# Kernel tuning notes

Measured on AMD Instinct MI355X. Metric: run time of the kernel, lower is better.

Reference implementation:

```python
import jax, jax.numpy as jnp
from jax import lax
import numpy as np

NUM_FEATURES = 30_000_000
NB_LABELS = 11  # 9 real tags + BOS + EOS
BOS, EOS = 9, 10
SEQ_LEN = 8192
N_ACTIVE = 14


def _make_transitions(key):
    t = jax.random.uniform(key, (NB_LABELS, NB_LABELS), minval=-0.1, maxval=0.1, dtype=jnp.float32)
    # hardcoded structural constraints from init_weights
    t = t.at[0:3, 4].set(-10.0).at[4:, 4].set(-10.0)
    t = t.at[0:1, 6].set(-10.0).at[2:, 6].set(-10.0)
    t = t.at[0:2, 7].set(-10.0).at[3:, 7].set(-10.0)
    t = t.at[0:5, 8].set(-10.0).at[6:, 8].set(-10.0)
    t = t.at[:, BOS].set(-10000.0)
    t = t.at[EOS, :].set(-10000.0)
    return t


def setup_inputs() -> dict:
    key = jax.random.key(0)
    k1, k2, k3 = jax.random.split(key, 3)
    x = jax.random.randint(k1, (SEQ_LEN, NB_LABELS, N_ACTIVE), 0, NUM_FEATURES, dtype=jnp.int64)
    # original inits emission weights to exactly 1.0; add tiny noise for a non-degenerate test
    emission_w = 1.0 + 0.01 * jax.random.normal(k2, (NUM_FEATURES,), dtype=jnp.float32)
    transitions = _make_transitions(k3)
    return {"x": x, "emission_w": emission_w, "transitions": transitions}


def reference(x, emission_w, transitions):
    # emissions: sparse feature-hashing sum == gather + sum over the 14 active indices
    emissions = emission_w[x].sum(-1)[None]  # (1, T, NB_LABELS)

    alphas0 = transitions[BOS][None] + emissions[:, 0]  # (1, L)

    def step(alphas, e_t):  # e_t: (1, L)
        # scores[b, prev, cur] = alphas[b, prev] + transitions[prev, cur] + e_t[b, cur]
        scores = alphas[:, :, None] + transitions[None] + e_t[:, None, :]
        return jnp.max(scores, axis=1), jnp.argmax(scores, axis=1)

    xs = jnp.swapaxes(emissions, 0, 1)[1:]  # (T-1, 1, L)
    alphas, bps = lax.scan(step, alphas0, xs)  # bps: (T-1, 1, L)

    end_scores = alphas + transitions[:, EOS][None]
    max_final_scores = jnp.max(end_scores, axis=1)  # (1,)
    final_tag = jnp.argmax(end_scores, axis=1)  # (1,)

    def back(tag, bp):  # tag: (1,), bp: (1, L)
        prev = bp[0][tag]
        return prev, prev

    _, earlier = lax.scan(back, final_tag, bps, reverse=True)  # (T-1, 1); earlier[t] = tag at time t
    path = jnp.concatenate([earlier[:, 0], final_tag])  # (T,)

    # sequential BIO-style path fixup, carrying the *corrected* previous tag
    def fix(prev, cur):
        new = cur
        new = jnp.where((cur == 4) & (prev != 3) & (prev != 4), 3, new)
        new = jnp.where((cur == 6) & (prev != 1) & (prev != 6), 1, new)
        new = jnp.where((cur == 7) & (prev != 2) & (prev != 7), 2, new)
        new = jnp.where((cur == 8) & (prev != 5) & (prev != 8), 5, new)
        return new, new

    _, fixed = lax.scan(fix, path[0], path[1:])
    path = jnp.concatenate([path[:1], fixed])
    return max_final_scores, path
```

## Files before the change

### kernel.cpp

```cpp
#include <hip/hip_runtime.h>
#include <stdint.h>


#define SEQ 8192
#define L 11
#define NS 9
#define NACT 14
#define NCH 128
#define CS 64

#define RL(v, l) __int_as_float(__builtin_amdgcn_readlane(__float_as_int(v), (l)))

#define OFF_E9 0
#define OFF_M 295040
#define OFF_BD 336512
#define OFF_AL 341184
#define OFF_DUMP 341248
#define OFF_BP 342272

__global__ __launch_bounds__(256) void k_emissions(const int* __restrict__ x,
                                                   const float* __restrict__ w,
                                                   float* __restrict__ E9) {
  int idx = blockIdx.x * 256 + threadIdx.x;
  int t = idx / 9;
  int c = idx - t * 9;
  const int* xr = x + (t * L + c) * NACT;
  int id[NACT];
#pragma unroll
  for (int j = 0; j < 7; j++) {
    int2 v = ((const int2*)xr)[j];
    id[2 * j] = v.x;
    id[2 * j + 1] = v.y;
  }
  float wv[NACT];
#pragma unroll
  for (int j = 0; j < NACT; j++) wv[j] = w[id[j]];
  float s = ((wv[0] + wv[1]) + (wv[2] + wv[3])) + ((wv[4] + wv[5]) + (wv[6] + wv[7]));
  s += wv[8]; s += wv[9]; s += wv[10]; s += wv[11]; s += wv[12]; s += wv[13];
  E9[idx] = s;
}

__global__ __launch_bounds__(64) void k_chunkmat(const float* __restrict__ E9,
                                                 const float* __restrict__ T,
                                                 float* __restrict__ M) {
  const int k = blockIdx.x;
  const int i = threadIdx.x;
  const int ii = (i < NS) ? i : (NS - 1);
  const bool act = (i < NS);

  float Tm[NS][NS];
#pragma unroll
  for (int p = 0; p < NS; p++)
#pragma unroll
    for (int c = 0; c < NS; c++) Tm[p][c] = T[p * L + c];

  const int t0 = k * CS + 1;
  const int len = (k == NCH - 1) ? (CS - 1) : CS;
  const float* ep = E9 + t0 * NS;

  float row[NS];
  {
    float e0[NS];
#pragma unroll
    for (int c = 0; c < NS; c++) e0[c] = ep[c];
#pragma unroll
    for (int c = 0; c < NS; c++) row[c] = Tm[ii][c] + e0[c];
  }
  float ebuf[NS];
#pragma unroll
  for (int c = 0; c < NS; c++) ebuf[c] = ep[NS + c];

#pragma unroll 2
  for (int r = 1; r < len; ++r) {
    float nrow[NS];
#pragma unroll
    for (int c = 0; c < NS; c++) {
      float s0 = row[0] + Tm[0][c];
      float s1 = row[1] + Tm[1][c];
      float s2 = row[2] + Tm[2][c];
      float s3 = row[3] + Tm[3][c];
      float s4 = row[4] + Tm[4][c];
      float s5 = row[5] + Tm[5][c];
      float s6 = row[6] + Tm[6][c];
      float s7 = row[7] + Tm[7][c];
      float s8 = row[8] + Tm[8][c];
      float ma = fmaxf(fmaxf(s0, s1), s2);
      float mb = fmaxf(fmaxf(s3, s4), s5);
      float mc = fmaxf(fmaxf(s6, s7), s8);
      nrow[c] = fmaxf(fmaxf(ma, mb), mc) + ebuf[c];
    }
    if (r + 1 < len) {
#pragma unroll
      for (int c = 0; c < NS; c++) ebuf[c] = ep[(r + 1) * NS + c];
    }
#pragma unroll
    for (int c = 0; c < NS; c++) row[c] = nrow[c];
  }
  if (act) {
#pragma unroll
    for (int c = 0; c < NS; c++) M[k * 81 + ii * NS + c] = row[c];
  }
}

__global__ __launch_bounds__(64) void k_combine(const float* __restrict__ E9,
                                                const float* __restrict__ T,
                                                const float* __restrict__ M,
                                                float* __restrict__ BD) {
  const int c = threadIdx.x;
  const int cc = (c < NS) ? c : (NS - 1);
  const bool act = (c < NS);

  float bd = T[9 * L + cc] + E9[cc];
  if (act) BD[c] = bd;

  const float* mp = M + cc;
  float mb[4][NS];
#pragma unroll
  for (int j = 0; j < 4; ++j)
#pragma unroll
    for (int p = 0; p < NS; p++) mb[j][p] = mp[j * 81 + p * NS];

  for (int kk = 0; kk < NCH; kk += 4) {
#pragma unroll
    for (int j = 0; j < 4; ++j) {
      float s0 = RL(bd, 0) + mb[j][0];
      float s1 = RL(bd, 1) + mb[j][1];
      float s2 = RL(bd, 2) + mb[j][2];
      float s3 = RL(bd, 3) + mb[j][3];
      float s4 = RL(bd, 4) + mb[j][4];
      float s5 = RL(bd, 5) + mb[j][5];
      float s6 = RL(bd, 6) + mb[j][6];
      float s7 = RL(bd, 7) + mb[j][7];
      float s8 = RL(bd, 8) + mb[j][8];
      float ma = fmaxf(fmaxf(s0, s1), s2);
      float mbv = fmaxf(fmaxf(s3, s4), s5);
      float mc = fmaxf(fmaxf(s6, s7), s8);
      bd = fmaxf(fmaxf(ma, mbv), mc);
      if (act) BD[(kk + j + 1) * NS + c] = bd;
      int nk = kk + 4 + j;
      if (nk > NCH - 1) nk = NCH - 1;
#pragma unroll
      for (int p = 0; p < NS; p++) mb[j][p] = mp[nk * 81 + p * NS];
    }
  }
}

__global__ __launch_bounds__(64) void k_replay(const float* __restrict__ E9,
                                               const float* __restrict__ T,
                                               const float* __restrict__ BD,
                                               unsigned char* __restrict__ bp9,
                                               unsigned char* __restrict__ dump,
                                               float* __restrict__ AL) {
  const int k = blockIdx.x;
  const int c = threadIdx.x;
  const int cc = (c < NS) ? c : (NS - 1);
  const bool act = (c < NS);

  float Tcol[NS];
#pragma unroll
  for (int p = 0; p < NS; p++) Tcol[p] = T[p * L + cc];

  const int t0 = k * CS + 1;
  const float* ep = E9 + t0 * NS + cc;
  unsigned char* bps = act ? (bp9 + t0 * NS + c) : (dump + c);

  float anew = BD[k * NS + cc];

  float evb[8];
#pragma unroll
  for (int j = 0; j < 8; ++j) evb[j] = ep[j * NS];
  const float* eload = ep + 8 * NS;

#define VSTEP(evv, bptr)                          \
  {                                               \
    float best = RL(anew, 0) + Tcol[0];           \
    int bi = 0;                                   \
    for (int p = 1; p < NS; ++p) {                \
      float sc = RL(anew, p) + Tcol[p];           \
      if (sc > best) { best = sc; bi = p; }       \
    }                                             \
    anew = best + (evv);                          \
    *(bptr) = (unsigned char)bi;                  \
  }

  const int ngrp = (k == NCH - 1) ? 7 : 8;
  for (int g = 0; g < ngrp; ++g) {
#pragma unroll
    for (int j = 0; j < 8; ++j) {
      float ev = evb[j];
      evb[j] = eload[j * NS];
      VSTEP(ev, bps + j * NS);
    }
    eload += 8 * NS;
    bps += 8 * NS;
  }
  if (k == NCH - 1) {
#pragma unroll
    for (int j = 0; j < 7; ++j) {
      float ev = evb[j];
      VSTEP(ev, bps + j * NS);
    }
    if (act) AL[c] = anew;
  }
#undef VSTEP
}

#define IDMAP 0x876543210ULL

__device__ __forceinline__ uint32_t mapply(uint64_t m, uint32_t s) {
  return (uint32_t)(m >> (s * 4)) & 15u;
}
__device__ __forceinline__ uint64_t mcompose(uint64_t A, uint64_t B) {
  uint64_t r = 0;
#pragma unroll
  for (int s = 0; s < 9; ++s) {
    uint32_t bs = (uint32_t)(B >> (4 * s)) & 15u;
    uint32_t as = (uint32_t)(A >> (4 * bs)) & 15u;
    r |= (uint64_t)as << (4 * s);
  }
  return r;
}
__device__ __forceinline__ uint64_t shup(uint64_t v, int d) {
  return (uint64_t)__shfl_up((long long)v, d);
}

__global__ __launch_bounds__(1024) void k_back(const unsigned char* __restrict__ gbp,
                                               const float* __restrict__ AL,
                                               const float* __restrict__ T,
                                               float* __restrict__ out) {
  __shared__ unsigned char raw[SEQ];
  __shared__ uint64_t wagg[16];
  __shared__ uint64_t wincl[16];
  __shared__ int ftag_s;
  const int tid = threadIdx.x;
  const int lane = tid & 63, wv = tid >> 6;

  if (tid == 0) {
    float best = AL[0] + T[10];
    int bt = 0;
#pragma unroll
    for (int p = 1; p < NS; ++p) {
      float s = AL[p] + T[p * L + 10];
      if (s > best) { best = s; bt = p; }
    }
    out[0] = best;
    ftag_s = bt;
    raw[SEQ - 1] = (unsigned char)bt;
  }

  uint64_t Lj[8];
  {
    uint64_t Lc = IDMAP;
#pragma unroll
    for (int j = 0; j < 8; ++j) {
      int r = 8 * tid + j + 1;
      int t = SEQ - r;
      uint64_t m = IDMAP;
      if (t >= 1) {
        const unsigned char* bpr = gbp + t * NS;
        uint64_t mm = 0;
#pragma unroll
        for (int s = 0; s < 9; ++s) mm |= (uint64_t)(bpr[s] & 15u) << (4 * s);
        m = mm;
      }
      Lc = mcompose(m, Lc);
      Lj[j] = Lc;
    }
  }
  uint64_t acc = Lj[7];
#pragma unroll
  for (int d = 1; d < 64; d <<= 1) {
    uint64_t v = shup(acc, d);
    if (lane >= d) acc = mcompose(acc, v);
  }
  if (lane == 63) wagg[wv] = acc;
  __syncthreads();
  if (wv == 0) {
    uint64_t a2 = (lane < 16) ? wagg[lane] : IDMAP;
#pragma unroll
    for (int d = 1; d < 16; d <<= 1) {
      uint64_t v = shup(a2, d);
      if (lane >= d) a2 = mcompose(a2, v);
    }
    if (lane < 16) wincl[lane] = a2;
  }
  __syncthreads();
  {
    uint64_t iex = shup(acc, 1);
    uint32_t s0 = (uint32_t)ftag_s;
    if (wv > 0) s0 = mapply(wincl[wv - 1], s0);
    if (lane > 0) s0 = mapply(iex, s0);
#pragma unroll
    for (int j = 0; j < 8; ++j) {
      int r = 8 * tid + j + 1;
      if (r <= SEQ - 1) raw[SEQ - 1 - r] = (unsigned char)mapply(Lj[j], s0);
    }
  }
  __syncthreads();

  uint64_t Fj[8];
  {
    uint64_t Fc = IDMAP;
#pragma unroll
    for (int j = 0; j < 8; ++j) {
      int t = 8 * tid + j + 1;
      uint64_t m = IDMAP;
      if (t <= SEQ - 1) {
        uint32_t cur = raw[t];
        uint64_t cm = 0x111111111ULL * (uint64_t)cur;
        if (cur == 4) cm = 0x333344333ULL;
        else if (cur == 6) cm = 0x116111161ULL;
        else if (cur == 7) cm = 0x272222722ULL;
        else if (cur == 8) cm = 0x855855555ULL;
        m = cm;
      }
      Fc = mcompose(m, Fc);
      Fj[j] = Fc;
    }
  }
  uint64_t acc2 = Fj[7];
#pragma unroll
  for (int d = 1; d < 64; d <<= 1) {
    uint64_t v = shup(acc2, d);
    if (lane >= d) acc2 = mcompose(acc2, v);
  }
  if (lane == 63) wagg[wv] = acc2;
  __syncthreads();
  if (wv == 0) {
    uint64_t a2 = (lane < 16) ? wagg[lane] : IDMAP;
#pragma unroll
    for (int d = 1; d < 16; d <<= 1) {
      uint64_t v = shup(a2, d);
      if (lane >= d) a2 = mcompose(a2, v);
    }
    if (lane < 16) wincl[lane] = a2;
  }
  __syncthreads();
  {
    uint64_t iex = shup(acc2, 1);
    uint32_t p0 = raw[0];
    if (wv > 0) p0 = mapply(wincl[wv - 1], p0);
    if (lane > 0) p0 = mapply(iex, p0);
#pragma unroll
    for (int j = 0; j < 8; ++j) {
      int t = 8 * tid + j + 1;
      if (t <= SEQ - 1) out[1 + t] = (float)mapply(Fj[j], p0);
    }
  }
  if (tid == 0) out[1] = (float)raw[0];
}

extern "C" void kernel_launch(void* const* d_in, const int* in_sizes, int n_in,
                              void* d_out, int out_size, void* d_ws, size_t ws_size,
                              hipStream_t stream) {
  const int* x = (const int*)d_in[0];
  const float* w = (const float*)d_in[1];
  const float* T = (const float*)d_in[2];
  float* out = (float*)d_out;
  char* ws = (char*)d_ws;
  float* E9 = (float*)(ws + OFF_E9);
  float* M = (float*)(ws + OFF_M);
  float* BD = (float*)(ws + OFF_BD);
  float* AL = (float*)(ws + OFF_AL);
  unsigned char* dump = (unsigned char*)(ws + OFF_DUMP);
  unsigned char* bp9 = (unsigned char*)(ws + OFF_BP);

  hipLaunchKernelGGL(k_emissions, dim3(SEQ * NS / 256), dim3(256), 0, stream, x, w, E9);
  hipLaunchKernelGGL(k_chunkmat, dim3(NCH), dim3(64), 0, stream, E9, T, M);
  hipLaunchKernelGGL(k_combine, dim3(1), dim3(64), 0, stream, E9, T, M, BD);
  hipLaunchKernelGGL(k_replay, dim3(NCH), dim3(64), 0, stream, E9, T, BD, bp9, dump, AL);
  hipLaunchKernelGGL(k_back, dim3(1), dim3(1024), 0, stream, bp9, AL, T, out);
}
```

Before: 103.7 us.

## Spread chunk max-plus matrix rows across lanes with shuffles; shrink combine prefetch depth

The chunk-matrix kernel used to have each of 9 threads compute a full 9-wide row serially with 81 add/max ops per step. Now 81 (row, column) entries are spread over two wavefronts, one lane each, and the previous row values are exchanged via __shfl. This cuts per-thread serial work on the critical recurrence but adds 9 cross-lane shuffles per step. The combine kernel's prefetch is also reduced from 4 chunks to 2, and launch bounds gain a min-blocks hint.

```diff
diff --git a/kernel.cpp b/kernel.cpp
--- a/kernel.cpp
+++ b/kernel.cpp
@@ -40,117 +40,119 @@
   E9[idx] = s;
 }
 
-__global__ __launch_bounds__(64) void k_chunkmat(const float* __restrict__ E9,
-                                                 const float* __restrict__ T,
-                                                 float* __restrict__ M) {
+__global__ __launch_bounds__(128, 1) void k_chunkmat(const float* __restrict__ E9,
+                                                     const float* __restrict__ T,
+                                                     float* __restrict__ M) {
   const int k = blockIdx.x;
-  const int i = threadIdx.x;
+  const int tid = threadIdx.x;
+  const int wvi = tid >> 6;
+  const int lane = tid & 63;
+  const int g = lane / 9;
+  const int c = lane - g * 9;
+  const int i = (wvi == 0) ? g : 7 + g;
+  const bool act = (wvi == 0) ? (lane < 63) : (lane < 18);
   const int ii = (i < NS) ? i : (NS - 1);
-  const bool act = (i < NS);
-
-  float Tm[NS][NS];
-#pragma unroll
-  for (int p = 0; p < NS; p++)
-#pragma unroll
-    for (int c = 0; c < NS; c++) Tm[p][c] = T[p * L + c];
+  const int gb = g * 9;
+
+  float Tc[NS];
+#pragma unroll
+  for (int p = 0; p < NS; p++) Tc[p] = T[p * L + c];
 
   const int t0 = k * CS + 1;
   const int len = (k == NCH - 1) ? (CS - 1) : CS;
-  const float* ep = E9 + t0 * NS;
-
-  float row[NS];
-  {
-    float e0[NS];
-#pragma unroll
-    for (int c = 0; c < NS; c++) e0[c] = ep[c];
-#pragma unroll
-    for (int c = 0; c < NS; c++) row[c] = Tm[ii][c] + e0[c];
-  }
-  float ebuf[NS];
-#pragma unroll
-  for (int c = 0; c < NS; c++) ebuf[c] = ep[NS + c];
-
-#pragma unroll 2
+  const float* ep = E9 + t0 * NS + c;
+
+  float v = T[ii * L + c] + ep[0];
+  float evn = ep[NS];
+
   for (int r = 1; r < len; ++r) {
-    float nrow[NS];
-#pragma unroll
-    for (int c = 0; c < NS; c++) {
-      float s0 = row[0] + Tm[0][c];
-      float s1 = row[1] + Tm[1][c];
-      float s2 = row[2] + Tm[2][c];
-      float s3 = row[3] + Tm[3][c];
-      float s4 = row[4] + Tm[4][c];
-      float s5 = row[5] + Tm[5][c];
-      float s6 = row[6] + Tm[6][c];
-      float s7 = row[7] + Tm[7][c];
-      float s8 = row[8] + Tm[8][c];
+    float ecur = evn;
+    evn = ep[(r + 1) * NS];
+    float s0 = __shfl(v, gb + 0) + Tc[0];
+    float s1 = __shfl(v, gb + 1) + Tc[1];
+    float s2 = __shfl(v, gb + 2) + Tc[2];
+    float s3 = __shfl(v, gb + 3) + Tc[3];
+    float s4 = __shfl(v, gb + 4) + Tc[4];
+    float s5 = __shfl(v, gb + 5) + Tc[5];
+    float s6 = __shfl(v, gb + 6) + Tc[6];
+    float s7 = __shfl(v, gb + 7) + Tc[7];
+    float s8 = __shfl(v, gb + 8) + Tc[8];
+    float ma = fmaxf(fmaxf(s0, s1), s2);
+    float mb = fmaxf(fmaxf(s3, s4), s5);
+    float mc = fmaxf(fmaxf(s6, s7), s8);
+    v = fmaxf(fmaxf(ma, mb), mc) + ecur;
+  }
+  if (act) M[k * 81 + i * NS + c] = v;
+}
+
+__global__ __launch_bounds__(64, 1) void k_combine(const float* __restrict__ E9,
+                                                   const float* __restrict__ T,
+                                                   const float* __restrict__ M,
+                                                   float* __restrict__ BD) {
+  const int c = threadIdx.x;
+  const int cc = (c < NS) ? c : (NS - 1);
+  const bool act = (c < NS);
+
+  float bd = T[9 * L + cc] + E9[cc];
+  if (act) BD[c] = bd;
+
+  const float* mp = M + cc;
+  float mA[NS], mB[NS];
+#pragma unroll
+  for (int p = 0; p < NS; p++) mA[p] = mp[p * NS];
+#pragma unroll
+  for (int p = 0; p < NS; p++) mB[p] = mp[81 + p * NS];
+
+  for (int kk = 0; kk < NCH; kk += 2) {
+    {
+      float s0 = RL(bd, 0) + mA[0];
+      float s1 = RL(bd, 1) + mA[1];
+      float s2 = RL(bd, 2) + mA[2];
+      float s3 = RL(bd, 3) + mA[3];
+      float s4 = RL(bd, 4) + mA[4];
+      float s5 = RL(bd, 5) + mA[5];
+      float s6 = RL(bd, 6) + mA[6];
+      float s7 = RL(bd, 7) + mA[7];
+      float s8 = RL(bd, 8) + mA[8];
       float ma = fmaxf(fmaxf(s0, s1), s2);
       float mb = fmaxf(fmaxf(s3, s4), s5);
       float mc = fmaxf(fmaxf(s6, s7), s8);
-      nrow[c] = fmaxf(fmaxf(ma, mb), mc) + ebuf[c];
-    }
-    if (r + 1 < len) {
-#pragma unroll
-      for (int c = 0; c < NS; c++) ebuf[c] = ep[(r + 1) * NS + c];
-    }
-#pragma unroll
-    for (int c = 0; c < NS; c++) row[c] = nrow[c];
-  }
-  if (act) {
-#pragma unroll
-    for (int c = 0; c < NS; c++) M[k * 81 + ii * NS + c] = row[c];
-  }
-}
-
-__global__ __launch_bounds__(64) void k_combine(const float* __restrict__ E9,
-                                                const float* __restrict__ T,
-                                                const float* __restrict__ M,
-                                                float* __restrict__ BD) {
-  const int c = threadIdx.x;
-  const int cc = (c < NS) ? c : (NS - 1);
-  const bool act = (c < NS);
-
-  float bd = T[9 * L + cc] + E9[cc];
-  if (act) BD[c] = bd;
-
-  const float* mp = M + cc;
-  float mb[4][NS];
-#pragma unroll
-  for (int j = 0; j < 4; ++j)
-#pragma unroll
-    for (int p = 0; p < NS; p++) mb[j][p] = mp[j * 81 + p * NS];
-
-  for (int kk = 0; kk < NCH; kk += 4) {
-#pragma unroll
-    for (int j = 0; j < 4; ++j) {
-      float s0 = RL(bd, 0) + mb[j][0];
-      float s1 = RL(bd, 1) + mb[j][1];
-      float s2 = RL(bd, 2) + mb[j][2];
-      float s3 = RL(bd, 3) + mb[j][3];
-      float s4 = RL(bd, 4) + mb[j][4];
-      float s5 = RL(bd, 5) + mb[j][5];
-      float s6 = RL(bd, 6) + mb[j][6];
-      float s7 = RL(bd, 7) + mb[j][7];
-      float s8 = RL(bd, 8) + mb[j][8];
+      bd = fmaxf(fmaxf(ma, mb), mc);
+      if (act) BD[(kk + 1) * NS + c] = bd;
+      int nk = kk + 2;
+      if (nk > NCH - 1) nk = NCH - 1;
+#pragma unroll
+      for (int p = 0; p < NS; p++) mA[p] = mp[nk * 81 + p * NS];
+    }
+    {
+      float s0 = RL(bd, 0) + mB[0];
+      float s1 = RL(bd, 1) + mB[1];
+      float s2 = RL(bd, 2) + mB[2];
+      float s3 = RL(bd, 3) + mB[3];
+      float s4 = RL(bd, 4) + mB[4];
+      float s5 = RL(bd, 5) + mB[5];
+      float s6 = RL(bd, 6) + mB[6];
+      float s7 = RL(bd, 7) + mB[7];
+      float s8 = RL(bd, 8) + mB[8];
       float ma = fmaxf(fmaxf(s0, s1), s2);
-      float mbv = fmaxf(fmaxf(s3, s4), s5);
+      float mb = fmaxf(fmaxf(s3, s4), s5);
       float mc = fmaxf(fmaxf(s6, s7), s8);
-      bd = fmaxf(fmaxf(ma, mbv), mc);
-      if (act) BD[(kk + j + 1) * NS + c] = bd;
-      int nk = kk + 4 + j;
+      bd = fmaxf(fmaxf(ma, mb), mc);
+      if (act) BD[(kk + 2) * NS + c] = bd;
+      int nk = kk + 3;
       if (nk > NCH - 1) nk = NCH - 1;
 #pragma unroll
-      for (int p = 0; p < NS; p++) mb[j][p] = mp[nk * 81 + p * NS];
-    }
-  }
-}
-
-__global__ __launch_bounds__(64) void k_replay(const float* __restrict__ E9,
-                                               const float* __restrict__ T,
-                                               const float* __restrict__ BD,
-                                               unsigned char* __restrict__ bp9,
-                                               unsigned char* __restrict__ dump,
-                                               float* __restrict__ AL) {
+      for (int p = 0; p < NS; p++) mB[p] = mp[nk * 81 + p * NS];
+    }
+  }
+}
+
+__global__ __launch_bounds__(64, 1) void k_replay(const float* __restrict__ E9,
+                                                  const float* __restrict__ T,
+                                                  const float* __restrict__ BD,
+                                                  unsigned char* __restrict__ bp9,
+                                                  unsigned char* __restrict__ dump,
+                                                  float* __restrict__ AL) {
   const int k = blockIdx.x;
   const int c = threadIdx.x;
   const int cc = (c < NS) ? c : (NS - 1);
@@ -366,7 +368,7 @@
   unsigned char* bp9 = (unsigned char*)(ws + OFF_BP);
 
   hipLaunchKernelGGL(k_emissions, dim3(SEQ * NS / 256), dim3(256), 0, stream, x, w, E9);
-  hipLaunchKernelGGL(k_chunkmat, dim3(NCH), dim3(64), 0, stream, E9, T, M);
+  hipLaunchKernelGGL(k_chunkmat, dim3(NCH), dim3(128), 0, stream, E9, T, M);
   hipLaunchKernelGGL(k_combine, dim3(1), dim3(64), 0, stream, E9, T, M, BD);
   hipLaunchKernelGGL(k_replay, dim3(NCH), dim3(64), 0, stream, E9, T, BD, bp9, dump, AL);
   hipLaunchKernelGGL(k_back, dim3(1), dim3(1024), 0, stream, bp9, AL, T, out);
```

Result: faster. 84.98 us (-18.1%).
